# Kernel tuning notes

Measured on AMD Instinct MI355X. Metric: run time of the kernel, lower is better.

The kernel has to match this reference:

```python
import jax, jax.numpy as jnp
import numpy as np

DIM = 1024          # d_model
DI = 2 * DIM        # d_inner (expand=2)
DSTATE = 16         # SSM state size
DCONV = 4           # causal conv width
DTRANK = DIM // 16  # dt_rank = ceil(dim/16) = 64
B_, L = 2, 2048


def setup_inputs() -> dict:
    key = jax.random.key(0)
    ks = jax.random.split(key, 8)
    s = lambda k, shape, sc=0.02: jax.random.normal(k, shape, jnp.float32) * sc
    return {
        "x": jax.random.normal(ks[0], (B_, L, DIM), jnp.float32),
        "ln_w": jnp.ones((DIM,), jnp.float32),
        "ln_b": jnp.zeros((DIM,), jnp.float32),
        "in_proj_w": s(ks[1], (2 * DI, DIM)),
        "conv_w": s(ks[2], (DI, 1, DCONV), 0.1),
        "conv_b": jnp.zeros((DI,), jnp.float32),
        "x_proj_w": s(ks[3], (DTRANK + 2 * DSTATE, DI)),
        "dt_proj_w": s(ks[4], (DI, DTRANK), 0.1),
        # standard Mamba dt bias init: softplus^{-1}(0.01)
        "dt_proj_b": jnp.log(jnp.expm1(jnp.full((DI,), 0.01, jnp.float32))),
        # S4D-real init: A = -[1..d_state]
        "A_log": jnp.log(jnp.broadcast_to(jnp.arange(1, DSTATE + 1, dtype=jnp.float32), (DI, DSTATE))),
        "D": jnp.ones((DI,), jnp.float32),
        "out_proj_w": s(ks[5], (DIM, DI)),
    }


def _layernorm(x, w, b, eps=1e-5):
    mu = x.mean(-1, keepdims=True)
    var = ((x - mu) ** 2).mean(-1, keepdims=True)
    return (x - mu) * jax.lax.rsqrt(var + eps) * w + b


def _silu(x):
    return x * jax.nn.sigmoid(x)


def _mamba(x, in_proj_w, conv_w, conv_b, x_proj_w, dt_proj_w, dt_proj_b, A_log, D, out_proj_w):
    b, l, _ = x.shape
    xz = x @ in_proj_w.T                      # [b,l,2*DI]
    xc, z = jnp.split(xz, 2, axis=-1)
    # depthwise causal conv over time
    xt = jnp.pad(xc.transpose(0, 2, 1), ((0, 0), (0, 0), (DCONV - 1, 0)))
    xt = jax.lax.conv_general_dilated(
        xt, conv_w, (1,), 'VALID',
        dimension_numbers=('NCH', 'OIH', 'NCH'), feature_group_count=DI)
    xc = _silu(xt + conv_b[None, :, None]).transpose(0, 2, 1)  # [b,l,DI]
    # input-dependent dt, B, C
    dbc = xc @ x_proj_w.T
    dt = dbc[..., :DTRANK]
    Bm = dbc[..., DTRANK:DTRANK + DSTATE]     # [b,l,n]
    Cm = dbc[..., DTRANK + DSTATE:]           # [b,l,n]
    delta = jax.nn.softplus(dt @ dt_proj_w.T + dt_proj_b)  # [b,l,DI]
    A = -jnp.exp(A_log)                        # [DI,n]
    dA = jnp.exp(delta[..., None] * A)         # [b,l,DI,n]
    dBu = (delta * xc)[..., None] * Bm[:, :, None, :]  # [b,l,DI,n]

    def step(h, inp):
        dA_t, dBu_t, C_t = inp
        h = dA_t * h + dBu_t                   # [b,DI,n]
        return h, jnp.einsum('bdn,bn->bd', h, C_t)

    h0 = jnp.zeros((b, DI, DSTATE), x.dtype)
    _, ys = jax.lax.scan(step, h0,
                         (dA.transpose(1, 0, 2, 3), dBu.transpose(1, 0, 2, 3), Cm.transpose(1, 0, 2)))
    y = ys.transpose(1, 0, 2) + xc * D         # [b,l,DI]
    y = y * _silu(z)
    return y @ out_proj_w.T


def reference(x, ln_w, ln_b, in_proj_w, conv_w, conv_b, x_proj_w, dt_proj_w, dt_proj_b, A_log, D, out_proj_w):
    # single block: x = x + Mamba(LN(x))
    return x + _mamba(_layernorm(x, ln_w, ln_b), in_proj_w, conv_w, conv_b,
                      x_proj_w, dt_proj_w, dt_proj_b, A_log, D, out_proj_w)
```

## Files before the change

### kernel.cpp

```cpp
#include <hip/hip_runtime.h>
#include <hip/hip_bf16.h>
#include <math.h>

#define DIM 1024
#define DI 2048
#define DSTATE 16
#define DTRANK 64
#define NB 2
#define L_ 2048
#define M_TOT (NB*L_)
#define NCHUNK 64
#define CLEN (L_/NCHUNK)

typedef unsigned short u16;
typedef float f32x4 __attribute__((ext_vector_type(4)));
typedef __bf16 bf16x8 __attribute__((ext_vector_type(8)));

static __device__ __forceinline__ float bf2f(u16 u){
  union{float f;unsigned int i;}x; x.i = ((unsigned int)u)<<16; return x.f;
}
static __device__ __forceinline__ u16 f2bf(float f){
  union{float f;unsigned int u;}v; v.f=f;
  unsigned int x = v.u;
  return (u16)((x + 0x7fffu + ((x>>16)&1u)) >> 16);
}
static __device__ __forceinline__ void gload16(const void* g, void* l){
  __builtin_amdgcn_global_load_lds(
      (const __attribute__((address_space(1))) unsigned int*)g,
      (__attribute__((address_space(3))) unsigned int*)l, 16, 0, 0);
}

#define N4_WIN  1048576
#define N4_WDT  32768
#define N4_WOUT 524288
__global__ void cast3_k(const float* __restrict__ s0, const float* __restrict__ s1,
                        const float* __restrict__ s2,
                        u16* __restrict__ o0, u16* __restrict__ o1, u16* __restrict__ o2){
  int i = blockIdx.x*256 + threadIdx.x;
  const float* s; u16* o; int j;
  if (i < N4_WIN){ s = s0; o = o0; j = i; }
  else if (i < N4_WIN+N4_WDT){ s = s1; o = o1; j = i - N4_WIN; }
  else { s = s2; o = o2; j = i - N4_WIN - N4_WDT; }
  float4 v = reinterpret_cast<const float4*>(s)[j];
  ushort4 ov; ov.x=f2bf(v.x); ov.y=f2bf(v.y); ov.z=f2bf(v.z); ov.w=f2bf(v.w);
  reinterpret_cast<ushort4*>(o)[j] = ov;
}

__global__ void cast_xproj_k(const float* __restrict__ src, u16* __restrict__ dst){
  int i = blockIdx.x*256 + threadIdx.x;
  int row = (i*4) >> 11;
  ushort4 o;
  if (row < 96){
    float4 v = reinterpret_cast<const float4*>(src)[i];
    o.x=f2bf(v.x); o.y=f2bf(v.y); o.z=f2bf(v.z); o.w=f2bf(v.w);
  } else { o.x=0;o.y=0;o.z=0;o.w=0; }
  reinterpret_cast<ushort4*>(dst)[i] = o;
}

__global__ __launch_bounds__(256) void ln_kernel(const float* __restrict__ x,
    const float* __restrict__ w, const float* __restrict__ b, u16* __restrict__ xn){
  const int row = blockIdx.x, t = threadIdx.x;
  const float4 v = reinterpret_cast<const float4*>(x + (size_t)row*DIM)[t];
  float s = v.x+v.y+v.z+v.w;
  float q = v.x*v.x+v.y*v.y+v.z*v.z+v.w*v.w;
  #pragma unroll
  for (int o=1;o<64;o<<=1){ s += __shfl_xor(s,o); q += __shfl_xor(q,o); }
  __shared__ float ss[4], sq[4];
  if ((t&63)==0){ ss[t>>6]=s; sq[t>>6]=q; }
  __syncthreads();
  s = ss[0]+ss[1]+ss[2]+ss[3]; q = sq[0]+sq[1]+sq[2]+sq[3];
  const float mu = s*(1.f/DIM);
  const float rs = rsqrtf(q*(1.f/DIM) - mu*mu + 1e-5f);
  const float4 wv = reinterpret_cast<const float4*>(w)[t];
  const float4 bv = reinterpret_cast<const float4*>(b)[t];
  ushort4 o;
  o.x = f2bf((v.x-mu)*rs*wv.x + bv.x);
  o.y = f2bf((v.y-mu)*rs*wv.y + bv.y);
  o.z = f2bf((v.z-mu)*rs*wv.z + bv.z);
  o.w = f2bf((v.w-mu)*rs*wv.w + bv.w);
  reinterpret_cast<ushort4*>(xn + (size_t)row*DIM)[t] = o;
}

template<int MODE, int NSPLIT>
__global__ __launch_bounds__(256,4) void gemm_bt(
    const u16* __restrict__ A, const u16* __restrict__ Bw, int K, int nbn, int nblk,
    float* __restrict__ f0,
    u16* __restrict__ b0, u16* __restrict__ b1,
    const float* __restrict__ e0){
  __shared__ u16 As[2][128*32];
  __shared__ u16 Bs[2][128*32];
  const int t = threadIdx.x;
  const int w = t >> 6, lane = t & 63;
  const int nwg = gridDim.x;
  int wg = blockIdx.x;
  wg = (wg & 7)*(nwg >> 3) + (wg >> 3);
  const int ks  = (NSPLIT > 1) ? (wg / nblk) : 0;
  const int rem = (NSPLIT > 1) ? (wg % nblk) : wg;
  const int bm = rem / nbn, bn = rem % nbn;
  const int row0 = bm*128, col0 = bn*128;
  const int wr = (w>>1)*64, wc = (w&1)*64;
  const int Kpart = K / NSPLIT;
  const int kbase = ks * Kpart;
  const int nt = Kpart >> 5;

  const int schunk = ((t&3) ^ ((t>>3)&3))*8;
  const u16* gA0 = A + (size_t)(row0 + (t>>2))*K + kbase + schunk;
  const u16* gA1 = gA0 + (size_t)64*K;
  const u16* gB0 = Bw + (size_t)(col0 + (t>>2))*K + kbase + schunk;
  const u16* gB1 = gB0 + (size_t)64*K;

  f32x4 acc[4][4];
  #pragma unroll
  for (int m=0;m<4;m++)
    #pragma unroll
    for (int n=0;n<4;n++) acc[m][n] = (f32x4){0.f,0.f,0.f,0.f};

  const int lrow = lane & 15;
  const int rchunk = ((lane>>4) ^ ((lane>>1)&3))*8;

  {
    char* a  = (char*)As[0] + (w<<10);
    char* bb = (char*)Bs[0] + (w<<10);
    gload16(gA0, a);  gload16(gA1, a + 4096);
    gload16(gB0, bb); gload16(gB1, bb + 4096);
    gA0 += 32; gA1 += 32; gB0 += 32; gB1 += 32;
  }
  __syncthreads();

  for (int it = 0; it < nt; ++it){
    const int cur = it & 1;
    if (it + 1 < nt){
      char* a  = (char*)As[cur^1] + (w<<10);
      char* bb = (char*)Bs[cur^1] + (w<<10);
      gload16(gA0, a);  gload16(gA1, a + 4096);
      gload16(gB0, bb); gload16(gB1, bb + 4096);
      gA0 += 32; gA1 += 32; gB0 += 32; gB1 += 32;
    }
    bf16x8 af[4], bfr[4];
    #pragma unroll
    for (int m=0;m<4;m++)
      af[m] = *reinterpret_cast<const bf16x8*>(&As[cur][(wr + m*16 + lrow)*32 + rchunk]);
    #pragma unroll
    for (int n=0;n<4;n++)
      bfr[n] = *reinterpret_cast<const bf16x8*>(&Bs[cur][(wc + n*16 + lrow)*32 + rchunk]);
    #pragma unroll
    for (int m=0;m<4;m++)
      #pragma unroll
      for (int n=0;n<4;n++)
        acc[m][n] = __builtin_amdgcn_mfma_f32_16x16x32_bf16(af[m], bfr[n], acc[m][n], 0,0,0);
    __syncthreads();
  }

  const int rb = (lane>>4)*4;
  #pragma unroll
  for (int m=0;m<4;m++){
    #pragma unroll
    for (int n=0;n<4;n++){
      #pragma unroll
      for (int i=0;i<4;i++){
        const int row = row0 + wr + m*16 + rb + i;
        const int col = col0 + wc + n*16 + lrow;
        const float v = acc[m][n][i];
        if (MODE==1){
          if (col < DI) b0[(size_t)row*DI + col] = f2bf(v);
          else          b1[(size_t)row*DI + col - DI] = f2bf(v);
        } else if (MODE==3){
          const float xv = v + e0[col];
          const float sp = (xv > 20.f) ? xv : log1pf(__expf(xv));
          b0[(size_t)row*DI + col] = f2bf(sp);
        } else if (MODE==5){
          f0[((size_t)ks*M_TOT + row)*128 + col] = v;
        } else {
          f0[((size_t)ks*M_TOT + row)*1024 + col] = v;
        }
      }
    }
  }
}

__global__ __launch_bounds__(256) void reduce_xp_k(const float* __restrict__ P,
    float* __restrict__ dbc, u16* __restrict__ dtb){
  const int tid = blockIdx.x*256 + threadIdx.x;
  const int m = tid >> 5, c4 = tid & 31;
  f32x4 s = (f32x4){0.f,0.f,0.f,0.f};
  #pragma unroll
  for (int k=0;k<8;k++)
    s += *reinterpret_cast<const f32x4*>(&P[((size_t)k*M_TOT + m)*128 + c4*4]);
  *reinterpret_cast<f32x4*>(&dbc[(size_t)m*128 + c4*4]) = s;
  if (c4 < 16){
    ushort4 o; o.x=f2bf(s.x); o.y=f2bf(s.y); o.z=f2bf(s.z); o.w=f2bf(s.w);
    *reinterpret_cast<ushort4*>(&dtb[(size_t)m*DTRANK + c4*4]) = o;
  }
}

__global__ __launch_bounds__(256) void reduce_out_k(const float* __restrict__ P,
    const float* __restrict__ x, float* __restrict__ out){
  const size_t i = ((size_t)blockIdx.x*256 + threadIdx.x)*4;
  f32x4 a = *reinterpret_cast<const f32x4*>(&P[i]);
  f32x4 b = *reinterpret_cast<const f32x4*>(&P[(size_t)M_TOT*1024 + i]);
  f32x4 xv = *reinterpret_cast<const f32x4*>(&x[i]);
  *reinterpret_cast<f32x4*>(&out[i]) = a + b + xv;
}

__global__ __launch_bounds__(256) void conv_silu_k(const u16* __restrict__ xc,
    const float* __restrict__ cw, const float* __restrict__ cb, u16* __restrict__ out){
  const int idx = blockIdx.x*256 + threadIdx.x;
  const int m = idx >> 9;
  const int dq = idx & 511;
  const int d0 = dq*4;
  const int l = m & (L_-1);
  float wgt[4][4];
  #pragma unroll
  for (int j=0;j<4;j++){
    float4 t4 = reinterpret_cast<const float4*>(cw)[d0+j];
    wgt[j][0]=t4.x; wgt[j][1]=t4.y; wgt[j][2]=t4.z; wgt[j][3]=t4.w;
  }
  const float4 bb = reinterpret_cast<const float4*>(cb)[dq];
  float acc[4] = {bb.x, bb.y, bb.z, bb.w};
  #pragma unroll
  for (int k=0;k<4;k++){
    const int ls = l + k - 3;
    if (ls >= 0){
      ushort4 xv = *reinterpret_cast<const ushort4*>(&xc[(size_t)(m+k-3)*DI + d0]);
      float xf[4] = {bf2f(xv.x), bf2f(xv.y), bf2f(xv.z), bf2f(xv.w)};
      #pragma unroll
      for (int j=0;j<4;j++) acc[j] += xf[j]*wgt[j][k];
    }
  }
  ushort4 o;
  u16 ov[4];
  #pragma unroll
  for (int j=0;j<4;j++){
    const float v = acc[j];
    ov[j] = f2bf(v / (1.f + __expf(-v)));
  }
  o.x=ov[0]; o.y=ov[1]; o.z=ov[2]; o.w=ov[3];
  *reinterpret_cast<ushort4*>(&out[(size_t)m*DI + d0]) = o;
}

__global__ __launch_bounds__(256) void scan1_k(const u16* __restrict__ delta,
    const u16* __restrict__ xc, const float* __restrict__ dbc,
    const float* __restrict__ A_log, float* __restrict__ aps, float* __restrict__ hend){
  const int bid = blockIdx.x;
  const int dblk = bid & 7;
  const int bc = bid >> 3;
  const int b = bc >> 6, c = bc & (NCHUNK-1);
  const int t = threadIdx.x;
  const int d = dblk*256 + t;
  __shared__ float Bsh[CLEN*DSTATE];
  const int mbase = b*L_ + c*CLEN;
  Bsh[t]     = dbc[(size_t)(mbase + (t>>4))*128 + 64 + (t&15)];
  Bsh[t+256] = dbc[(size_t)(mbase + 16 + (t>>4))*128 + 64 + (t&15)];
  float un[DSTATE], h[DSTATE];
  #pragma unroll
  for (int n=0;n<DSTATE;n++){
    un[n] = -__expf(A_log[d*DSTATE + n]);
    h[n] = 0.f;
  }
  __syncthreads();
  const u16* dp = delta + (size_t)mbase*DI + d;
  const u16* xp = xc    + (size_t)mbase*DI + d;
  float sdv = 0.f;
  u16 dr = dp[0];
  u16 xr = xp[0];
  for (int j=0;j<CLEN;j++){
    const int jn = (j+1 < CLEN) ? j+1 : j;
    const u16 dr_n = dp[(size_t)jn*DI];
    const u16 xr_n = xp[(size_t)jn*DI];
    const float dv = bf2f(dr);
    const float xf = bf2f(xr);
    sdv += dv;
    const float c0 = dv * xf;
    #pragma unroll
    for (int n=0;n<DSTATE;n++){
      const float dA = __expf(un[n]*dv);
      h[n] = fmaf(dA, h[n], c0 * Bsh[j*DSTATE+n]);
    }
    dr = dr_n; xr = xr_n;
  }
  float* ap_out = aps  + (size_t)bc*(DSTATE*DI) + d;
  float* he_out = hend + (size_t)bc*(DSTATE*DI) + d;
  #pragma unroll
  for (int n=0;n<DSTATE;n++){
    ap_out[(size_t)n*DI] = __expf(un[n]*sdv);
    he_out[(size_t)n*DI] = h[n];
  }
}

__global__ void combine_k(const float* __restrict__ aps, const float* __restrict__ hend,
                          float* __restrict__ hinit){
  const int gid = blockIdx.x*256 + threadIdx.x;
  const int b = gid >> 15;
  const int dn = gid & 32767;
  float h = 0.f;
  #pragma unroll 4
  for (int c=0;c<NCHUNK;c++){
    const size_t idx = (size_t)(b*NCHUNK + c)*(DI*DSTATE) + dn;
    hinit[idx] = h;
    h = hend[idx] + aps[idx]*h;
  }
}

__global__ __launch_bounds__(256) void scan2_k(const u16* __restrict__ delta,
    const u16* __restrict__ xc, const float* __restrict__ dbc,
    const u16* __restrict__ z, const float* __restrict__ A_log, const float* __restrict__ Dvec,
    const float* __restrict__ hinit, u16* __restrict__ y){
  const int bid = blockIdx.x;
  const int dblk = bid & 7;
  const int bc = bid >> 3;
  const int b = bc >> 6, c = bc & (NCHUNK-1);
  const int t = threadIdx.x;
  const int d = dblk*256 + t;
  __shared__ float Bsh[CLEN*DSTATE], Csh[CLEN*DSTATE];
  const int mbase = b*L_ + c*CLEN;
  Bsh[t]     = dbc[(size_t)(mbase + (t>>4))*128 + 64 + (t&15)];
  Bsh[t+256] = dbc[(size_t)(mbase + 16 + (t>>4))*128 + 64 + (t&15)];
  Csh[t]     = dbc[(size_t)(mbase + (t>>4))*128 + 80 + (t&15)];
  Csh[t+256] = dbc[(size_t)(mbase + 16 + (t>>4))*128 + 80 + (t&15)];
  float un[DSTATE], h[DSTATE];
  const float* hi = hinit + (size_t)bc*(DSTATE*DI) + d;
  #pragma unroll
  for (int n=0;n<DSTATE;n++){
    un[n] = -__expf(A_log[d*DSTATE+n]);
    h[n] = hi[(size_t)n*DI];
  }
  const float Dd = Dvec[d];
  __syncthreads();
  const u16* dp = delta + (size_t)mbase*DI + d;
  const u16* xp = xc    + (size_t)mbase*DI + d;
  const u16* zp = z     + (size_t)mbase*DI + d;
  u16* yp = y + (size_t)mbase*DI + d;
  u16 dr = dp[0];
  u16 xr = xp[0], zr = zp[0];
  for (int j=0;j<CLEN;j++){
    const int jn = (j+1 < CLEN) ? j+1 : j;
    const u16 dr_n = dp[(size_t)jn*DI];
    const u16 xr_n = xp[(size_t)jn*DI];
    const u16 zr_n = zp[(size_t)jn*DI];
    const float dv = bf2f(dr);
    const float xf = bf2f(xr), zf = bf2f(zr);
    const float c0 = dv * xf;
    float s = 0.f;
    #pragma unroll
    for (int n=0;n<DSTATE;n++){
      const float dA = __expf(un[n]*dv);
      h[n] = fmaf(dA, h[n], c0 * Bsh[j*DSTATE+n]);
      s = fmaf(h[n], Csh[j*DSTATE+n], s);
    }
    const float yf = fmaf(xf, Dd, s);
    const float yo = yf * (zf / (1.f + __expf(-zf)));
    yp[(size_t)j*DI] = f2bf(yo);
    dr = dr_n; xr = xr_n; zr = zr_n;
  }
}

extern "C" void kernel_launch(void* const* d_in, const int* in_sizes, int n_in,
                              void* d_out, int out_size, void* d_ws, size_t ws_size,
                              hipStream_t stream){
  const float* x         = (const float*)d_in[0];
  const float* ln_w      = (const float*)d_in[1];
  const float* ln_b      = (const float*)d_in[2];
  const float* in_proj_w = (const float*)d_in[3];
  const float* conv_w    = (const float*)d_in[4];
  const float* conv_b    = (const float*)d_in[5];
  const float* x_proj_w  = (const float*)d_in[6];
  const float* dt_proj_w = (const float*)d_in[7];
  const float* dt_proj_b = (const float*)d_in[8];
  const float* A_log     = (const float*)d_in[9];
  const float* Dvec      = (const float*)d_in[10];
  const float* out_proj_w= (const float*)d_in[11];
  float* out = (float*)d_out;

  char* w = (char*)d_ws;
  size_t off = 0;
  auto carve = [&](size_t bytes)->char*{ char* p = w + off; off += (bytes + 255) & ~(size_t)255; return p; };
  u16*   xn    = (u16*)  carve((size_t)M_TOT*DIM*2);
  u16*   win   = (u16*)  carve((size_t)2*DI*DIM*2);
  u16*   xcb   = (u16*)  carve((size_t)M_TOT*DI*2);
  u16*   zb    = (u16*)  carve((size_t)M_TOT*DI*2);
  u16*   xcv   = (u16*)  carve((size_t)M_TOT*DI*2);
  u16*   wxp   = (u16*)  carve((size_t)128*DI*2);
  u16*   dtb   = (u16*)  carve((size_t)M_TOT*DTRANK*2);
  u16*   wdt   = (u16*)  carve((size_t)DI*DTRANK*2);
  u16*   deltab= (u16*)  carve((size_t)M_TOT*DI*2);
  u16*   wout  = (u16*)  carve((size_t)DIM*DI*2);
  u16*   yb    = (u16*)  carve((size_t)M_TOT*DI*2);
  float* Pxp   = (float*)carve((size_t)8*M_TOT*128*4);
  float* dbc   = (float*)carve((size_t)M_TOT*128*4);
  float* aps   = (float*)carve((size_t)NB*NCHUNK*DI*DSTATE*4);
  float* hend  = (float*)carve((size_t)NB*NCHUNK*DI*DSTATE*4);
  float* hinit = (float*)carve((size_t)NB*NCHUNK*DI*DSTATE*4);
  float* Pout  = (float*)xcb;

  cast3_k<<<(N4_WIN+N4_WDT+N4_WOUT)/256, 256, 0, stream>>>(in_proj_w, dt_proj_w, out_proj_w,
                                                           win, wdt, wout);
  cast_xproj_k<<<256, 256, 0, stream>>>(x_proj_w, wxp);

  ln_kernel<<<M_TOT, 256, 0, stream>>>(x, ln_w, ln_b, xn);

  gemm_bt<1,1><<<32*32, 256, 0, stream>>>(xn, win, DIM, 32, 1024, nullptr, xcb, zb, nullptr);

  conv_silu_k<<<(M_TOT*512)/256, 256, 0, stream>>>(xcb, conv_w, conv_b, xcv);

  gemm_bt<5,8><<<32*8, 256, 0, stream>>>(xcv, wxp, DI, 1, 32, Pxp, nullptr, nullptr, nullptr);
  reduce_xp_k<<<(M_TOT*32)/256, 256, 0, stream>>>(Pxp, dbc, dtb);

  gemm_bt<3,1><<<32*16, 256, 0, stream>>>(dtb, wdt, DTRANK, 16, 512, nullptr, deltab, nullptr, dt_proj_b);

  scan1_k<<<NB*NCHUNK*8, 256, 0, stream>>>(deltab, xcv, dbc, A_log, aps, hend);
  combine_k<<<(NB*DI*DSTATE)/256, 256, 0, stream>>>(aps, hend, hinit);
  scan2_k<<<NB*NCHUNK*8, 256, 0, stream>>>(deltab, xcv, dbc, zb, A_log, Dvec, hinit, yb);

  gemm_bt<6,2><<<2*32*8, 256, 0, stream>>>(yb, wout, DI, 8, 256, Pout, nullptr, nullptr, nullptr);
  reduce_out_k<<<(M_TOT*1024)/(4*256), 256, 0, stream>>>(Pout, x, out);
}
```

Before: 249.7 us.

## Use 4-stage LDS ring GEMM, fuse prologue kernels, bf16 out-proj partials

The GEMM moves from a double buffer to a 4-deep LDS ring buffer with explicit vmcnt waits and a single barrier per K step. The goal is to hide global-load latency behind MFMA work, at the cost of more LDS and lower occupancy (launch bounds drop from 4 to 2). The weight casts and layernorm are merged into one launch to save kernel-launch overhead. Out-proj split-K partials are stored as bf16 instead of fp32, which halves that traffic but loses precision in the reduction.

Result: no change. 248.9 us (-0.3%).

```diff
diff --git a/kernel.cpp b/kernel.cpp
--- a/kernel.cpp
+++ b/kernel.cpp
@@ -33,33 +33,39 @@
 #define N4_WIN  1048576
 #define N4_WDT  32768
 #define N4_WOUT 524288
-__global__ void cast3_k(const float* __restrict__ s0, const float* __restrict__ s1,
-                        const float* __restrict__ s2,
-                        u16* __restrict__ o0, u16* __restrict__ o1, u16* __restrict__ o2){
-  int i = blockIdx.x*256 + threadIdx.x;
-  const float* s; u16* o; int j;
-  if (i < N4_WIN){ s = s0; o = o0; j = i; }
-  else if (i < N4_WIN+N4_WDT){ s = s1; o = o1; j = i - N4_WIN; }
-  else { s = s2; o = o2; j = i - N4_WIN - N4_WDT; }
-  float4 v = reinterpret_cast<const float4*>(s)[j];
-  ushort4 ov; ov.x=f2bf(v.x); ov.y=f2bf(v.y); ov.z=f2bf(v.z); ov.w=f2bf(v.w);
-  reinterpret_cast<ushort4*>(o)[j] = ov;
-}
-
-__global__ void cast_xproj_k(const float* __restrict__ src, u16* __restrict__ dst){
-  int i = blockIdx.x*256 + threadIdx.x;
-  int row = (i*4) >> 11;
-  ushort4 o;
-  if (row < 96){
-    float4 v = reinterpret_cast<const float4*>(src)[i];
-    o.x=f2bf(v.x); o.y=f2bf(v.y); o.z=f2bf(v.z); o.w=f2bf(v.w);
-  } else { o.x=0;o.y=0;o.z=0;o.w=0; }
-  reinterpret_cast<ushort4*>(dst)[i] = o;
-}
-
-__global__ __launch_bounds__(256) void ln_kernel(const float* __restrict__ x,
-    const float* __restrict__ w, const float* __restrict__ b, u16* __restrict__ xn){
-  const int row = blockIdx.x, t = threadIdx.x;
+#define NB_CAST3 ((N4_WIN+N4_WDT+N4_WOUT)/256)
+#define NB_XPROJ 256
+#define NB_LN    M_TOT
+__global__ __launch_bounds__(256) void fused_pre_k(
+    const float* __restrict__ in_proj_w, const float* __restrict__ dt_proj_w,
+    const float* __restrict__ out_proj_w, const float* __restrict__ x_proj_w,
+    const float* __restrict__ x, const float* __restrict__ lw, const float* __restrict__ lb,
+    u16* __restrict__ win, u16* __restrict__ wdt, u16* __restrict__ wout,
+    u16* __restrict__ wxp, u16* __restrict__ xn){
+  const int bid = blockIdx.x, t = threadIdx.x;
+  if (bid < NB_CAST3){
+    int i = bid*256 + t;
+    const float* s; u16* o; int j;
+    if (i < N4_WIN){ s = in_proj_w; o = win; j = i; }
+    else if (i < N4_WIN+N4_WDT){ s = dt_proj_w; o = wdt; j = i - N4_WIN; }
+    else { s = out_proj_w; o = wout; j = i - N4_WIN - N4_WDT; }
+    float4 v = reinterpret_cast<const float4*>(s)[j];
+    ushort4 ov; ov.x=f2bf(v.x); ov.y=f2bf(v.y); ov.z=f2bf(v.z); ov.w=f2bf(v.w);
+    reinterpret_cast<ushort4*>(o)[j] = ov;
+    return;
+  }
+  if (bid < NB_CAST3 + NB_XPROJ){
+    int i = (bid - NB_CAST3)*256 + t;
+    int row = (i*4) >> 11;
+    ushort4 o;
+    if (row < 96){
+      float4 v = reinterpret_cast<const float4*>(x_proj_w)[i];
+      o.x=f2bf(v.x); o.y=f2bf(v.y); o.z=f2bf(v.z); o.w=f2bf(v.w);
+    } else { o.x=0;o.y=0;o.z=0;o.w=0; }
+    reinterpret_cast<ushort4*>(wxp)[i] = o;
+    return;
+  }
+  const int row = bid - NB_CAST3 - NB_XPROJ;
   const float4 v = reinterpret_cast<const float4*>(x + (size_t)row*DIM)[t];
   float s = v.x+v.y+v.z+v.w;
   float q = v.x*v.x+v.y*v.y+v.z*v.z+v.w*v.w;
@@ -71,8 +77,8 @@
   s = ss[0]+ss[1]+ss[2]+ss[3]; q = sq[0]+sq[1]+sq[2]+sq[3];
   const float mu = s*(1.f/DIM);
   const float rs = rsqrtf(q*(1.f/DIM) - mu*mu + 1e-5f);
-  const float4 wv = reinterpret_cast<const float4*>(w)[t];
-  const float4 bv = reinterpret_cast<const float4*>(b)[t];
+  const float4 wv = reinterpret_cast<const float4*>(lw)[t];
+  const float4 bv = reinterpret_cast<const float4*>(lb)[t];
   ushort4 o;
   o.x = f2bf((v.x-mu)*rs*wv.x + bv.x);
   o.y = f2bf((v.y-mu)*rs*wv.y + bv.y);
@@ -82,32 +88,39 @@
 }
 
 template<int MODE, int NSPLIT>
-__global__ __launch_bounds__(256,4) void gemm_bt(
+__global__ __launch_bounds__(256,2) void ring_gemm(
     const u16* __restrict__ A, const u16* __restrict__ Bw, int K, int nbn, int nblk,
-    float* __restrict__ f0,
-    u16* __restrict__ b0, u16* __restrict__ b1,
+    float* __restrict__ f0, u16* __restrict__ b0, u16* __restrict__ b1,
     const float* __restrict__ e0){
-  __shared__ u16 As[2][128*32];
-  __shared__ u16 Bs[2][128*32];
+  constexpr int BM = 128;
+  constexpr int TILE_ELEMS = BM*32;
+  constexpr int BUF_BYTES = TILE_ELEMS*2*2;
+  __shared__ u16 lds0[4*2*TILE_ELEMS];
   const int t = threadIdx.x;
   const int w = t >> 6, lane = t & 63;
+  const int lrow = lane & 15;
   const int nwg = gridDim.x;
   int wg = blockIdx.x;
   wg = (wg & 7)*(nwg >> 3) + (wg >> 3);
   const int ks  = (NSPLIT > 1) ? (wg / nblk) : 0;
   const int rem = (NSPLIT > 1) ? (wg % nblk) : wg;
   const int bm = rem / nbn, bn = rem % nbn;
-  const int row0 = bm*128, col0 = bn*128;
+  const int row0 = bm*BM, col0 = bn*BM;
   const int wr = (w>>1)*64, wc = (w&1)*64;
   const int Kpart = K / NSPLIT;
   const int kbase = ks * Kpart;
   const int nt = Kpart >> 5;
 
+  const int srow = t >> 2;
   const int schunk = ((t&3) ^ ((t>>3)&3))*8;
-  const u16* gA0 = A + (size_t)(row0 + (t>>2))*K + kbase + schunk;
+  const u16* gA0 = A + (size_t)(row0 + srow)*K + kbase + schunk;
   const u16* gA1 = gA0 + (size_t)64*K;
-  const u16* gB0 = Bw + (size_t)(col0 + (t>>2))*K + kbase + schunk;
+  const u16* gB0 = Bw + (size_t)(col0 + srow)*K + kbase + schunk;
   const u16* gB1 = gB0 + (size_t)64*K;
+  const int baseA0 = (w*16)*64;
+  const int baseA1 = (64 + w*16)*64;
+  const int baseB0 = BM*64 + baseA0;
+  const int baseB1 = BM*64 + baseA1;
 
   f32x4 acc[4][4];
   #pragma unroll
@@ -115,40 +128,40 @@
     #pragma unroll
     for (int n=0;n<4;n++) acc[m][n] = (f32x4){0.f,0.f,0.f,0.f};
 
-  const int lrow = lane & 15;
   const int rchunk = ((lane>>4) ^ ((lane>>1)&3))*8;
 
-  {
-    char* a  = (char*)As[0] + (w<<10);
-    char* bb = (char*)Bs[0] + (w<<10);
-    gload16(gA0, a);  gload16(gA1, a + 4096);
-    gload16(gB0, bb); gload16(gB1, bb + 4096);
+  for (int p = 0; p < 3 && p < nt; ++p){
+    char* bp = (char*)lds0 + p*BUF_BYTES;
+    gload16(gA0, bp + baseA0); gload16(gA1, bp + baseA1);
+    gload16(gB0, bp + baseB0); gload16(gB1, bp + baseB1);
     gA0 += 32; gA1 += 32; gB0 += 32; gB1 += 32;
   }
-  __syncthreads();
-
-  for (int it = 0; it < nt; ++it){
-    const int cur = it & 1;
-    if (it + 1 < nt){
-      char* a  = (char*)As[cur^1] + (w<<10);
-      char* bb = (char*)Bs[cur^1] + (w<<10);
-      gload16(gA0, a);  gload16(gA1, a + 4096);
-      gload16(gB0, bb); gload16(gB1, bb + 4096);
+
+  for (int t2 = 0; t2 < nt; ++t2){
+    const int left = nt - 1 - t2;
+    if (left >= 2)      asm volatile("s_waitcnt vmcnt(8)" ::: "memory");
+    else if (left == 1) asm volatile("s_waitcnt vmcnt(4)" ::: "memory");
+    else                asm volatile("s_waitcnt vmcnt(0)" ::: "memory");
+    __builtin_amdgcn_s_barrier();
+    if (t2 + 3 < nt){
+      char* bp = (char*)lds0 + ((t2+3)&3)*BUF_BYTES;
+      gload16(gA0, bp + baseA0); gload16(gA1, bp + baseA1);
+      gload16(gB0, bp + baseB0); gload16(gB1, bp + baseB1);
       gA0 += 32; gA1 += 32; gB0 += 32; gB1 += 32;
     }
-    bf16x8 af[4], bfr[4];
+    const u16* Lb = (const u16*)((const char*)lds0 + (t2&3)*BUF_BYTES);
+    bf16x8 af[4], bfv[4];
     #pragma unroll
     for (int m=0;m<4;m++)
-      af[m] = *reinterpret_cast<const bf16x8*>(&As[cur][(wr + m*16 + lrow)*32 + rchunk]);
+      af[m] = *reinterpret_cast<const bf16x8*>(&Lb[(wr + m*16 + lrow)*32 + rchunk]);
     #pragma unroll
     for (int n=0;n<4;n++)
-      bfr[n] = *reinterpret_cast<const bf16x8*>(&Bs[cur][(wc + n*16 + lrow)*32 + rchunk]);
+      bfv[n] = *reinterpret_cast<const bf16x8*>(&Lb[TILE_ELEMS + (wc + n*16 + lrow)*32 + rchunk]);
     #pragma unroll
     for (int m=0;m<4;m++)
       #pragma unroll
       for (int n=0;n<4;n++)
-        acc[m][n] = __builtin_amdgcn_mfma_f32_16x16x32_bf16(af[m], bfr[n], acc[m][n], 0,0,0);
-    __syncthreads();
+        acc[m][n] = __builtin_amdgcn_mfma_f32_16x16x32_bf16(af[m], bfv[n], acc[m][n], 0,0,0);
   }
 
   const int rb = (lane>>4)*4;
@@ -171,7 +184,7 @@
         } else if (MODE==5){
           f0[((size_t)ks*M_TOT + row)*128 + col] = v;
         } else {
-          f0[((size_t)ks*M_TOT + row)*1024 + col] = v;
+          b0[((size_t)ks*M_TOT + row)*1024 + col] = f2bf(v);
         }
       }
     }
@@ -193,13 +206,18 @@
   }
 }
 
-__global__ __launch_bounds__(256) void reduce_out_k(const float* __restrict__ P,
+__global__ __launch_bounds__(256) void reduce_out_k(const u16* __restrict__ P,
     const float* __restrict__ x, float* __restrict__ out){
   const size_t i = ((size_t)blockIdx.x*256 + threadIdx.x)*4;
-  f32x4 a = *reinterpret_cast<const f32x4*>(&P[i]);
-  f32x4 b = *reinterpret_cast<const f32x4*>(&P[(size_t)M_TOT*1024 + i]);
+  ushort4 a = *reinterpret_cast<const ushort4*>(&P[i]);
+  ushort4 b = *reinterpret_cast<const ushort4*>(&P[(size_t)M_TOT*1024 + i]);
   f32x4 xv = *reinterpret_cast<const f32x4*>(&x[i]);
-  *reinterpret_cast<f32x4*>(&out[i]) = a + b + xv;
+  f32x4 r;
+  r.x = bf2f(a.x) + bf2f(b.x) + xv.x;
+  r.y = bf2f(a.y) + bf2f(b.y) + xv.y;
+  r.z = bf2f(a.z) + bf2f(b.z) + xv.z;
+  r.w = bf2f(a.w) + bf2f(b.w) + xv.w;
+  *reinterpret_cast<f32x4*>(&out[i]) = r;
 }
 
 __global__ __launch_bounds__(256) void conv_silu_k(const u16* __restrict__ xc,
@@ -390,27 +408,25 @@
   float* aps   = (float*)carve((size_t)NB*NCHUNK*DI*DSTATE*4);
   float* hend  = (float*)carve((size_t)NB*NCHUNK*DI*DSTATE*4);
   float* hinit = (float*)carve((size_t)NB*NCHUNK*DI*DSTATE*4);
-  float* Pout  = (float*)xcb;
-
-  cast3_k<<<(N4_WIN+N4_WDT+N4_WOUT)/256, 256, 0, stream>>>(in_proj_w, dt_proj_w, out_proj_w,
-                                                           win, wdt, wout);
-  cast_xproj_k<<<256, 256, 0, stream>>>(x_proj_w, wxp);
-
-  ln_kernel<<<M_TOT, 256, 0, stream>>>(x, ln_w, ln_b, xn);
-
-  gemm_bt<1,1><<<32*32, 256, 0, stream>>>(xn, win, DIM, 32, 1024, nullptr, xcb, zb, nullptr);
+  u16* Pout = xcb;
+
+  fused_pre_k<<<NB_CAST3 + NB_XPROJ + NB_LN, 256, 0, stream>>>(
+      in_proj_w, dt_proj_w, out_proj_w, x_proj_w, x, ln_w, ln_b,
+      win, wdt, wout, wxp, xn);
+
+  ring_gemm<1,1><<<32*32, 256, 0, stream>>>(xn, win, DIM, 32, 1024, nullptr, xcb, zb, nullptr);
 
   conv_silu_k<<<(M_TOT*512)/256, 256, 0, stream>>>(xcb, conv_w, conv_b, xcv);
 
-  gemm_bt<5,8><<<32*8, 256, 0, stream>>>(xcv, wxp, DI, 1, 32, Pxp, nullptr, nullptr, nullptr);
+  ring_gemm<5,8><<<8*32, 256, 0, stream>>>(xcv, wxp, DI, 1, 32, Pxp, nullptr, nullptr, nullptr);
   reduce_xp_k<<<(M_TOT*32)/256, 256, 0, stream>>>(Pxp, dbc, dtb);
 
-  gemm_bt<3,1><<<32*16, 256, 0, stream>>>(dtb, wdt, DTRANK, 16, 512, nullptr, deltab, nullptr, dt_proj_b);
+  ring_gemm<3,1><<<32*16, 256, 0, stream>>>(dtb, wdt, DTRANK, 16, 512, nullptr, deltab, nullptr, dt_proj_b);
 
   scan1_k<<<NB*NCHUNK*8, 256, 0, stream>>>(deltab, xcv, dbc, A_log, aps, hend);
   combine_k<<<(NB*DI*DSTATE)/256, 256, 0, stream>>>(aps, hend, hinit);
   scan2_k<<<NB*NCHUNK*8, 256, 0, stream>>>(deltab, xcv, dbc, zb, A_log, Dvec, hinit, yb);
 
-  gemm_bt<6,2><<<2*32*8, 256, 0, stream>>>(yb, wout, DI, 8, 256, Pout, nullptr, nullptr, nullptr);
+  ring_gemm<6,2><<<2*32*8, 256, 0, stream>>>(yb, wout, DI, 8, 256, nullptr, Pout, nullptr, nullptr);
   reduce_out_k<<<(M_TOT*1024)/(4*256), 256, 0, stream>>>(Pout, x, out);
 }
```
